# Kernel optimization log

Hardware: AMD Instinct MI355X
Metric: run time of the kernel (lower is better)

Reference implementation:

```python
import jax, jax.numpy as jnp
import numpy as np

D_MODEL = 1024
N_HEADS = 16
D_K = D_MODEL // N_HEADS
EPS = 1e-8


def _l2_rownorm(x):
    # RowNormActivation: normalize each row (last dim) to unit L2 norm
    return x * jax.lax.rsqrt(jnp.sum(x * x, axis=-1, keepdims=True) + EPS)


def setup_inputs() -> dict:
    key = jax.random.key(0)
    ks = jax.random.split(key, 11)
    B, S = 2, 2048
    sc = 1.0 / np.sqrt(D_MODEL)
    inp = {
        "Q": jax.random.normal(ks[0], (B, S, D_MODEL), jnp.float32),
        "K": jax.random.normal(ks[1], (B, S, D_MODEL), jnp.float32),
        "V": jax.random.normal(ks[2], (B, S, D_MODEL), jnp.float32),
        "Wq_w": jax.random.normal(ks[3], (D_MODEL, D_MODEL), jnp.float32) * sc,
        "Wq_b": jnp.zeros((D_MODEL,), jnp.float32),
        "Wk_w": jax.random.normal(ks[4], (D_MODEL, D_MODEL), jnp.float32) * sc,
        "Wk_b": jnp.zeros((D_MODEL,), jnp.float32),
        "Wv_w": jax.random.normal(ks[5], (D_MODEL, D_MODEL), jnp.float32) * sc,
        "Wv_b": jnp.zeros((D_MODEL,), jnp.float32),
        "Wo_w": jax.random.normal(ks[6], (D_MODEL, D_MODEL), jnp.float32) * sc,
        "Wo_b": jnp.zeros((D_MODEL,), jnp.float32),
    }
    return inp


def reference(Q, K, V, Wq_w, Wq_b, Wk_w, Wk_b, Wv_w, Wv_b, Wo_w, Wo_b):
    B, S, _ = Q.shape
    # torch Linear: y = x @ W.T + b
    q = (Q @ Wq_w.T + Wq_b).reshape(B, S, N_HEADS, D_K).transpose(0, 2, 1, 3)
    k = (K @ Wk_w.T + Wk_b).reshape(B, S, N_HEADS, D_K).transpose(0, 2, 1, 3)
    v = (V @ Wv_w.T + Wv_b).reshape(B, S, N_HEADS, D_K).transpose(0, 2, 1, 3)
    qn = _l2_rownorm(q)
    kn = _l2_rownorm(k)
    scores = jnp.einsum("bhqd,bhkd->bhqk", qn, kn)
    attn = scores * scores  # squared similarity, no softmax (dropout=0 / eval)
    out = jnp.einsum("bhqk,bhkd->bhqd", attn, v)
    out = out.transpose(0, 2, 1, 3).reshape(B, S, D_MODEL)
    return out @ Wo_w.T + Wo_b
```

## Files before the change

### kernel.cpp

```cpp
#include <hip/hip_runtime.h>


#define D_MODEL 1024
#define N_HEADS 16
#define D_K     64
#define BATCH   2
#define SEQ     2048
#define M_TOT   (BATCH * SEQ)

typedef short  s16x8 __attribute__((ext_vector_type(8)));
typedef float  f32x4 __attribute__((ext_vector_type(4)));
typedef unsigned short ushort_t;
typedef ushort_t us4 __attribute__((ext_vector_type(4)));

__device__ __forceinline__ ushort_t f2bf(float f) {
    union { float f; unsigned int u; } x; x.f = f;
    unsigned int u = x.u;
    return (ushort_t)((u + 0x7fffu + ((u >> 16) & 1u)) >> 16);
}
__device__ __forceinline__ float bf2f(ushort_t h) {
    union { unsigned int u; float f; } x; x.u = ((unsigned int)h) << 16;
    return x.f;
}

__device__ __forceinline__ void gload_lds16(const ushort_t* g, ushort_t* l) {
    __builtin_amdgcn_global_load_lds(
        (__attribute__((address_space(1))) void*)(ushort_t*)g,
        (__attribute__((address_space(3))) void*)l, 16, 0, 0);
}

#define WAIT_VM(n)  asm volatile("s_waitcnt vmcnt(" #n ")" ::: "memory")
#define WAIT_LGKM0  asm volatile("s_waitcnt lgkmcnt(0)" ::: "memory")
#define BARRIER     asm volatile("s_barrier" ::: "memory")

struct ConvArgs {
    const float* src[11];
    ushort_t*    dst[11];
    int          n[11];
};

__global__ __launch_bounds__(256) void convert_kernel(ConvArgs a) {
    const int t = blockIdx.y;
    const int i = (blockIdx.x * 256 + threadIdx.x) * 4;
    if (i >= a.n[t]) return;
    const float4 v = *(const float4*)(a.src[t] + i);
    us4 p;
    p[0] = f2bf(v.x); p[1] = f2bf(v.y); p[2] = f2bf(v.z); p[3] = f2bf(v.w);
    *(us4*)(a.dst[t] + i) = p;
}

template <int BM, int MODE>
__device__ __forceinline__ void gemm_body(
    ushort_t* __restrict__ smem,
    const ushort_t* __restrict__ A,
    const ushort_t* __restrict__ W,
    const ushort_t* __restrict__ bias,
    ushort_t* __restrict__ out,
    float* __restrict__ outf,
    int bx, int by)
{
    static_assert(BM == 64 || BM == 128, "");
    constexpr int K    = 1024;
    constexpr int MF   = BM / 32;
    constexpr int BUFW = (BM + 128) * 64;
    constexpr int NIT  = K / 64;

    const int t    = threadIdx.x;
    const int wave = t >> 6;
    const int lane = t & 63;
    const int quad = lane >> 4;
    const int lc   = lane & 15;
    const int wm   = wave >> 1;
    const int wn   = wave & 1;
    const int m0   = bx * BM;
    const int n0   = by * 128;

    f32x4 acc[MF][4];
    const f32x4 zero = {0.f, 0.f, 0.f, 0.f};
#pragma unroll
    for (int i = 0; i < MF; ++i)
#pragma unroll
        for (int j = 0; j < 4; ++j) acc[i][j] = zero;

    auto stage = [&](int buf, int k0) {
        ushort_t* Ast = smem + buf * BUFW;
        ushort_t* Bst = Ast + BM * 64;
#pragma unroll
        for (int c = 0; c < MF; ++c) {
            int idx = c * 256 + t;
            int row = idx >> 3, phys = idx & 7;
            int col = (phys ^ (row & 7)) * 8;
            gload_lds16(A + (size_t)(m0 + row) * K + k0 + col, Ast + idx * 8);
        }
#pragma unroll
        for (int c = 0; c < 4; ++c) {
            int idx = c * 256 + t;
            int row = idx >> 3, phys = idx & 7;
            int col = (phys ^ (row & 7)) * 8;
            gload_lds16(W + (size_t)(n0 + row) * K + k0 + col, Bst + idx * 8);
        }
    };
    auto comp = [&](int buf) {
        ushort_t* Ast = smem + buf * BUFW;
        ushort_t* Bst = Ast + BM * 64;
#pragma unroll
        for (int ks = 0; ks < 2; ++ks) {
            const int ph = ((ks * 4 + quad) ^ (lc & 7)) * 8;
            s16x8 a[MF], b[4];
#pragma unroll
            for (int i = 0; i < MF; ++i)
                a[i] = *(const s16x8*)(Ast + (wm * (BM / 2) + i * 16 + lc) * 64 + ph);
#pragma unroll
            for (int i = 0; i < 4; ++i)
                b[i] = *(const s16x8*)(Bst + (wn * 64 + i * 16 + lc) * 64 + ph);
#pragma unroll
            for (int mf = 0; mf < MF; ++mf)
#pragma unroll
                for (int nf = 0; nf < 4; ++nf)
                    acc[mf][nf] = __builtin_amdgcn_mfma_f32_16x16x32_bf16(
                        a[mf], b[nf], acc[mf][nf], 0, 0, 0);
        }
    };

    stage(0, 0);
    stage(1, 64);
    for (int it = 0; it < NIT - 2; ++it) {
        if constexpr (BM == 128) WAIT_VM(8); else WAIT_VM(6);
        BARRIER;
        comp(it & 1);
        WAIT_LGKM0;
        BARRIER;
        stage(it & 1, (it + 2) * 64);
    }
    if constexpr (BM == 128) WAIT_VM(8); else WAIT_VM(6);
    BARRIER;
    comp((NIT - 2) & 1);
    WAIT_VM(0);
    BARRIER;
    comp((NIT - 1) & 1);

    float bv[4];
#pragma unroll
    for (int nf = 0; nf < 4; ++nf) bv[nf] = bf2f(bias[n0 + wn * 64 + nf * 16 + lc]);

    if (MODE == 0) {
#pragma unroll
        for (int mf = 0; mf < MF; ++mf)
#pragma unroll
            for (int nf = 0; nf < 4; ++nf)
#pragma unroll
                for (int r = 0; r < 4; ++r) {
                    int mg = m0 + wm * (BM / 2) + mf * 16 + quad * 4 + r;
                    int ng = n0 + wn * 64 + nf * 16 + lc;
                    outf[(size_t)mg * D_MODEL + ng] = acc[mf][nf][r] + bv[nf];
                }
    } else if (MODE == 1) {
#pragma unroll
        for (int mf = 0; mf < MF; ++mf)
#pragma unroll
            for (int r = 0; r < 4; ++r) {
                float ss = 0.f;
#pragma unroll
                for (int nf = 0; nf < 4; ++nf) {
                    float v = acc[mf][nf][r] + bv[nf];
                    acc[mf][nf][r] = v;
                    ss += v * v;
                }
                ss += __shfl_xor(ss, 1);
                ss += __shfl_xor(ss, 2);
                ss += __shfl_xor(ss, 4);
                ss += __shfl_xor(ss, 8);
                float inv = rsqrtf(ss + 1e-8f);
                int mg = m0 + wm * (BM / 2) + mf * 16 + quad * 4 + r;
                int b  = mg >> 11;
                int s  = mg & 2047;
#pragma unroll
                for (int nf = 0; nf < 4; ++nf) {
                    int ng = n0 + wn * 64 + nf * 16 + lc;
                    int h = ng >> 6, d = ng & 63;
                    out[(((size_t)(b * N_HEADS + h)) * SEQ + s) * D_K + d] =
                        f2bf(acc[mf][nf][r] * inv);
                }
            }
    } else {
        __syncthreads();
        ushort_t* vt = smem + wave * (64 * 72);
#pragma unroll
        for (int mf = 0; mf < 4; ++mf)
#pragma unroll
            for (int nf = 0; nf < 4; ++nf) {
                us4 p;
#pragma unroll
                for (int r = 0; r < 4; ++r) p[r] = f2bf(acc[mf][nf][r] + bv[nf]);
                *(us4*)(vt + (nf * 16 + lc) * 72 + mf * 16 + quad * 4) = p;
            }
        WAIT_LGKM0;
#pragma unroll
        for (int r = 0; r < 8; ++r) {
            int d  = r * 8 + (lane >> 3);
            int so = (lane & 7) * 8;
            uint4 val = *(const uint4*)(vt + d * 72 + so);
            int mg = m0 + wm * 64 + so;
            int b  = mg >> 11;
            int s  = mg & 2047;
            int ng = n0 + wn * 64 + d;
            int h = ng >> 6, dh = ng & 63;
            *(uint4*)(out + (((size_t)(b * N_HEADS + h)) * D_K + dh) * SEQ + s) = val;
        }
    }
}

__global__ __launch_bounds__(256) void qkv_kernel(
    const ushort_t* __restrict__ Qb, const ushort_t* __restrict__ Kb,
    const ushort_t* __restrict__ Vb,
    const ushort_t* __restrict__ Wq, const ushort_t* __restrict__ Wk,
    const ushort_t* __restrict__ Wv,
    const ushort_t* __restrict__ bq, const ushort_t* __restrict__ bk,
    const ushort_t* __restrict__ bv,
    ushort_t* __restrict__ qn, ushort_t* __restrict__ kn,
    ushort_t* __restrict__ vT)
{
    __shared__ __align__(16) ushort_t smem[2 * (128 + 128) * 64];
    const int z = blockIdx.z;
    if (z == 0)
        gemm_body<128, 1>(smem, Qb, Wq, bq, qn, nullptr, blockIdx.x, blockIdx.y);
    else if (z == 1)
        gemm_body<128, 1>(smem, Kb, Wk, bk, kn, nullptr, blockIdx.x, blockIdx.y);
    else
        gemm_body<128, 2>(smem, Vb, Wv, bv, vT, nullptr, blockIdx.x, blockIdx.y);
}

__global__ __launch_bounds__(256) void wo_kernel(
    const ushort_t* __restrict__ A, const ushort_t* __restrict__ W,
    const ushort_t* __restrict__ bias, float* __restrict__ outf)
{
    __shared__ __align__(16) ushort_t smem[2 * (64 + 128) * 64];
    gemm_body<64, 0>(smem, A, W, bias, nullptr, outf, blockIdx.x, blockIdx.y);
}

__global__ __launch_bounds__(256) void attn_kernel(
    const ushort_t* __restrict__ qn,
    const ushort_t* __restrict__ kn,
    const ushort_t* __restrict__ vT,
    ushort_t* __restrict__ attn_out)
{
    __shared__ __align__(16) ushort_t smem[2 * 8192 + 4 * 16 * 72];

    const int t    = threadIdx.x;
    const int wave = t >> 6;
    const int lane = t & 63;
    const int quad = lane >> 4;
    const int lc   = lane & 15;
    const int qt   = blockIdx.x;
    const int bh   = blockIdx.y;
    const int b    = bh >> 4;
    const int h    = bh & 15;

    const ushort_t* qb = qn + (size_t)bh * SEQ * D_K;
    const ushort_t* kb = kn + (size_t)bh * SEQ * D_K;
    const ushort_t* vb = vT + (size_t)bh * D_K * SEQ;
    const int q0 = qt * 64 + wave * 16;

    s16x8 aq[2];
#pragma unroll
    for (int ks = 0; ks < 2; ++ks)
        aq[ks] = *(const s16x8*)(qb + (size_t)(q0 + lc) * D_K + ks * 32 + quad * 8);

    f32x4 oacc[4];
    const f32x4 zero = {0.f, 0.f, 0.f, 0.f};
#pragma unroll
    for (int df = 0; df < 4; ++df) oacc[df] = zero;

    ushort_t* pl = smem + 2 * 8192 + wave * 16 * 72;

    auto stage = [&](int buf, int j0) {
        ushort_t* kst = smem + buf * 8192;
        ushort_t* vst = kst + 4096;
#pragma unroll
        for (int c = 0; c < 2; ++c) {
            int idx = c * 256 + t;
            int row = idx >> 3, phys = idx & 7;
            int col = (phys ^ (row & 7)) * 8;
            gload_lds16(kb + (size_t)(j0 + row) * D_K + col, kst + idx * 8);
            gload_lds16(vb + (size_t)row * SEQ + j0 + col, vst + idx * 8);
        }
    };
    auto comp = [&](int buf) {
        ushort_t* kst = smem + buf * 8192;
        ushort_t* vst = kst + 4096;
        const int ph0 = ((0 * 4 + quad) ^ (lc & 7)) * 8;
        const int ph1 = ((1 * 4 + quad) ^ (lc & 7)) * 8;
        s16x8 bk[4][2];
#pragma unroll
        for (int jf = 0; jf < 4; ++jf) {
            bk[jf][0] = *(const s16x8*)(kst + (jf * 16 + lc) * 64 + ph0);
            bk[jf][1] = *(const s16x8*)(kst + (jf * 16 + lc) * 64 + ph1);
        }
        f32x4 s[4];
#pragma unroll
        for (int jf = 0; jf < 4; ++jf) {
            s[jf] = zero;
#pragma unroll
            for (int ks = 0; ks < 2; ++ks)
                s[jf] = __builtin_amdgcn_mfma_f32_16x16x32_bf16(aq[ks], bk[jf][ks], s[jf], 0, 0, 0);
        }
#pragma unroll
        for (int jf = 0; jf < 4; ++jf)
#pragma unroll
            for (int r = 0; r < 4; ++r)
                pl[(quad * 4 + r) * 72 + jf * 16 + lc] = f2bf(s[jf][r] * s[jf][r]);
        s16x8 bvf[4][2];
#pragma unroll
        for (int df = 0; df < 4; ++df) {
            bvf[df][0] = *(const s16x8*)(vst + (df * 16 + lc) * 64 + ph0);
            bvf[df][1] = *(const s16x8*)(vst + (df * 16 + lc) * 64 + ph1);
        }
        WAIT_LGKM0;
        s16x8 aa[2];
#pragma unroll
        for (int ks = 0; ks < 2; ++ks)
            aa[ks] = *(const s16x8*)(pl + lc * 72 + ks * 32 + quad * 8);
#pragma unroll
        for (int df = 0; df < 4; ++df)
#pragma unroll
            for (int ks = 0; ks < 2; ++ks)
                oacc[df] = __builtin_amdgcn_mfma_f32_16x16x32_bf16(
                    aa[ks], bvf[df][ks], oacc[df], 0, 0, 0);
    };

    constexpr int NT = 32;
    stage(0, 0);
    stage(1, 64);
    for (int it = 0; it < NT - 2; ++it) {
        WAIT_VM(4);
        BARRIER;
        comp(it & 1);
        WAIT_LGKM0;
        BARRIER;
        stage(it & 1, (it + 2) * 64);
    }
    WAIT_VM(4);
    BARRIER;
    comp((NT - 2) & 1);
    WAIT_VM(0);
    BARRIER;
    comp((NT - 1) & 1);

#pragma unroll
    for (int df = 0; df < 4; ++df)
#pragma unroll
        for (int r = 0; r < 4; ++r) {
            int s = q0 + quad * 4 + r;
            int d = df * 16 + lc;
            attn_out[((size_t)(b * SEQ + s)) * D_MODEL + h * D_K + d] =
                f2bf(oacc[df][r]);
        }
}

extern "C" void kernel_launch(void* const* d_in, const int* in_sizes, int n_in,
                              void* d_out, int out_size, void* d_ws, size_t ws_size,
                              hipStream_t stream)
{
    const float* Qf   = (const float*)d_in[0];
    const float* Kf   = (const float*)d_in[1];
    const float* Vf   = (const float*)d_in[2];
    const float* Wqf  = (const float*)d_in[3];
    const float* Wqbf = (const float*)d_in[4];
    const float* Wkf  = (const float*)d_in[5];
    const float* Wkbf = (const float*)d_in[6];
    const float* Wvf  = (const float*)d_in[7];
    const float* Wvbf = (const float*)d_in[8];
    const float* Wof  = (const float*)d_in[9];
    const float* Wobf = (const float*)d_in[10];

    const size_t NM = (size_t)M_TOT * D_MODEL;
    const size_t NW = (size_t)D_MODEL * D_MODEL;
    const size_t NB = D_MODEL;

    ushort_t* p = (ushort_t*)d_ws;
    ushort_t* Qb  = p;  p += NM;
    ushort_t* Kb  = p;  p += NM;
    ushort_t* Vb  = p;  p += NM;
    ushort_t* Wq  = p;  p += NW;
    ushort_t* Wk  = p;  p += NW;
    ushort_t* Wv  = p;  p += NW;
    ushort_t* Wo  = p;  p += NW;
    ushort_t* bq  = p;  p += NB;
    ushort_t* bk  = p;  p += NB;
    ushort_t* bvv = p;  p += NB;
    ushort_t* bo  = p;  p += NB;
    ushort_t* qn  = p;  p += NM;
    ushort_t* kn  = p;  p += NM;
    ushort_t* vT  = p;  p += NM;
    ushort_t* ao  = p;  p += NM;

    ConvArgs ca;
    ca.src[0] = Qf;   ca.dst[0] = Qb;  ca.n[0] = (int)NM;
    ca.src[1] = Kf;   ca.dst[1] = Kb;  ca.n[1] = (int)NM;
    ca.src[2] = Vf;   ca.dst[2] = Vb;  ca.n[2] = (int)NM;
    ca.src[3] = Wqf;  ca.dst[3] = Wq;  ca.n[3] = (int)NW;
    ca.src[4] = Wkf;  ca.dst[4] = Wk;  ca.n[4] = (int)NW;
    ca.src[5] = Wvf;  ca.dst[5] = Wv;  ca.n[5] = (int)NW;
    ca.src[6] = Wof;  ca.dst[6] = Wo;  ca.n[6] = (int)NW;
    ca.src[7] = Wqbf; ca.dst[7] = bq;  ca.n[7] = (int)NB;
    ca.src[8] = Wkbf; ca.dst[8] = bk;  ca.n[8] = (int)NB;
    ca.src[9] = Wvbf; ca.dst[9] = bvv; ca.n[9] = (int)NB;
    ca.src[10] = Wobf; ca.dst[10] = bo; ca.n[10] = (int)NB;

    dim3 blk(256);
    convert_kernel<<<dim3((unsigned)(NM / (256 * 4)), 11), blk, 0, stream>>>(ca);

    qkv_kernel<<<dim3(M_TOT / 128, D_MODEL / 128, 3), blk, 0, stream>>>(
        Qb, Kb, Vb, Wq, Wk, Wv, bq, bk, bvv, qn, kn, vT);
    attn_kernel<<<dim3(SEQ / 64, BATCH * N_HEADS), blk, 0, stream>>>(qn, kn, vT, ao);
    wo_kernel<<<dim3(M_TOT / 64, D_MODEL / 128), blk, 0, stream>>>(
        ao, Wo, bo, (float*)d_out);
}
```

Measured before the change: 238.2 us.

## Double per-wave query rows in attention and vectorize score stores

Each attention wave now handles 32 query rows instead of 16, so every K/V tile staged in shared memory is reused across twice as many queries and global K/V traffic per query is halved. The QK MFMA operands are swapped so each lane holds four consecutive key scores, which lets the squared scores be packed into bf16 pairs and written with one 8-byte store instead of scalar stores. The grid is reordered to put batch-head on x and halved along the query dimension, so there are fewer blocks, more accumulator registers per wave, and less occupancy.

After: 243.7 us. 2.3% more time.

```diff
diff --git a/kernel.cpp b/kernel.cpp
--- a/kernel.cpp
+++ b/kernel.cpp
@@ -1,4 +1,5 @@
 #include <hip/hip_runtime.h>
+#include <hip/hip_bf16.h>
 
 
 #define D_MODEL 1024
@@ -21,6 +22,11 @@
 __device__ __forceinline__ float bf2f(ushort_t h) {
     union { unsigned int u; float f; } x; x.u = ((unsigned int)h) << 16;
     return x.f;
+}
+__device__ __forceinline__ unsigned int pack2bf(float a, float b) {
+    union { __hip_bfloat162 h; unsigned int u; } x;
+    x.h = __float22bfloat162_rn(float2{a, b});
+    return x.u;
 }
 
 __device__ __forceinline__ void gload_lds16(const ushort_t* g, ushort_t* l) {
@@ -244,34 +250,39 @@
     const ushort_t* __restrict__ vT,
     ushort_t* __restrict__ attn_out)
 {
-    __shared__ __align__(16) ushort_t smem[2 * 8192 + 4 * 16 * 72];
+    __shared__ __align__(16) ushort_t smem[2 * 8192 + 4 * 32 * 72];
 
     const int t    = threadIdx.x;
     const int wave = t >> 6;
     const int lane = t & 63;
     const int quad = lane >> 4;
     const int lc   = lane & 15;
-    const int qt   = blockIdx.x;
-    const int bh   = blockIdx.y;
+    const int bh   = blockIdx.x;
+    const int qt   = blockIdx.y;
     const int b    = bh >> 4;
     const int h    = bh & 15;
 
     const ushort_t* qb = qn + (size_t)bh * SEQ * D_K;
     const ushort_t* kb = kn + (size_t)bh * SEQ * D_K;
     const ushort_t* vb = vT + (size_t)bh * D_K * SEQ;
-    const int q0 = qt * 64 + wave * 16;
-
-    s16x8 aq[2];
-#pragma unroll
-    for (int ks = 0; ks < 2; ++ks)
-        aq[ks] = *(const s16x8*)(qb + (size_t)(q0 + lc) * D_K + ks * 32 + quad * 8);
-
-    f32x4 oacc[4];
+    const int q0 = qt * 128 + wave * 32;
+
+    s16x8 aq[2][2];
+#pragma unroll
+    for (int mf = 0; mf < 2; ++mf)
+#pragma unroll
+        for (int ks = 0; ks < 2; ++ks)
+            aq[mf][ks] = *(const s16x8*)(qb + (size_t)(q0 + mf * 16 + lc) * D_K +
+                                         ks * 32 + quad * 8);
+
+    f32x4 oacc[2][4];
     const f32x4 zero = {0.f, 0.f, 0.f, 0.f};
 #pragma unroll
-    for (int df = 0; df < 4; ++df) oacc[df] = zero;
-
-    ushort_t* pl = smem + 2 * 8192 + wave * 16 * 72;
+    for (int mf = 0; mf < 2; ++mf)
+#pragma unroll
+        for (int df = 0; df < 4; ++df) oacc[mf][df] = zero;
+
+    ushort_t* pl = smem + 2 * 8192 + wave * 32 * 72;
 
     auto stage = [&](int buf, int j0) {
         ushort_t* kst = smem + buf * 8192;
@@ -296,19 +307,28 @@
             bk[jf][0] = *(const s16x8*)(kst + (jf * 16 + lc) * 64 + ph0);
             bk[jf][1] = *(const s16x8*)(kst + (jf * 16 + lc) * 64 + ph1);
         }
-        f32x4 s[4];
-#pragma unroll
-        for (int jf = 0; jf < 4; ++jf) {
-            s[jf] = zero;
-#pragma unroll
-            for (int ks = 0; ks < 2; ++ks)
-                s[jf] = __builtin_amdgcn_mfma_f32_16x16x32_bf16(aq[ks], bk[jf][ks], s[jf], 0, 0, 0);
-        }
+        f32x4 s[4][2];
 #pragma unroll
         for (int jf = 0; jf < 4; ++jf)
 #pragma unroll
-            for (int r = 0; r < 4; ++r)
-                pl[(quad * 4 + r) * 72 + jf * 16 + lc] = f2bf(s[jf][r] * s[jf][r]);
+            for (int mf = 0; mf < 2; ++mf) {
+                s[jf][mf] = zero;
+#pragma unroll
+                for (int ks = 0; ks < 2; ++ks)
+                    s[jf][mf] = __builtin_amdgcn_mfma_f32_16x16x32_bf16(
+                        bk[jf][ks], aq[mf][ks], s[jf][mf], 0, 0, 0);
+            }
+#pragma unroll
+        for (int jf = 0; jf < 4; ++jf)
+#pragma unroll
+            for (int mf = 0; mf < 2; ++mf) {
+                float p0 = s[jf][mf][0] * s[jf][mf][0];
+                float p1 = s[jf][mf][1] * s[jf][mf][1];
+                float p2 = s[jf][mf][2] * s[jf][mf][2];
+                float p3 = s[jf][mf][3] * s[jf][mf][3];
+                uint2 w = {pack2bf(p0, p1), pack2bf(p2, p3)};
+                *(uint2*)(pl + (mf * 16 + lc) * 72 + jf * 16 + quad * 4) = w;
+            }
         s16x8 bvf[4][2];
 #pragma unroll
         for (int df = 0; df < 4; ++df) {
@@ -316,16 +336,21 @@
             bvf[df][1] = *(const s16x8*)(vst + (df * 16 + lc) * 64 + ph1);
         }
         WAIT_LGKM0;
-        s16x8 aa[2];
-#pragma unroll
-        for (int ks = 0; ks < 2; ++ks)
-            aa[ks] = *(const s16x8*)(pl + lc * 72 + ks * 32 + quad * 8);
-#pragma unroll
-        for (int df = 0; df < 4; ++df)
+        s16x8 aa[2][2];
+#pragma unroll
+        for (int mf = 0; mf < 2; ++mf)
 #pragma unroll
             for (int ks = 0; ks < 2; ++ks)
-                oacc[df] = __builtin_amdgcn_mfma_f32_16x16x32_bf16(
-                    aa[ks], bvf[df][ks], oacc[df], 0, 0, 0);
+                aa[mf][ks] = *(const s16x8*)(pl + (mf * 16 + lc) * 72 +
+                                             ks * 32 + quad * 8);
+#pragma unroll
+        for (int mf = 0; mf < 2; ++mf)
+#pragma unroll
+            for (int df = 0; df < 4; ++df)
+#pragma unroll
+                for (int ks = 0; ks < 2; ++ks)
+                    oacc[mf][df] = __builtin_amdgcn_mfma_f32_16x16x32_bf16(
+                        aa[mf][ks], bvf[df][ks], oacc[mf][df], 0, 0, 0);
     };
 
     constexpr int NT = 32;
@@ -347,14 +372,16 @@
     comp((NT - 1) & 1);
 
 #pragma unroll
-    for (int df = 0; df < 4; ++df)
-#pragma unroll
-        for (int r = 0; r < 4; ++r) {
-            int s = q0 + quad * 4 + r;
-            int d = df * 16 + lc;
-            attn_out[((size_t)(b * SEQ + s)) * D_MODEL + h * D_K + d] =
-                f2bf(oacc[df][r]);
-        }
+    for (int mf = 0; mf < 2; ++mf)
+#pragma unroll
+        for (int df = 0; df < 4; ++df)
+#pragma unroll
+            for (int r = 0; r < 4; ++r) {
+                int s = q0 + mf * 16 + quad * 4 + r;
+                int d = df * 16 + lc;
+                attn_out[((size_t)(b * SEQ + s)) * D_MODEL + h * D_K + d] =
+                    f2bf(oacc[mf][df][r]);
+            }
 }
 
 extern "C" void kernel_launch(void* const* d_in, const int* in_sizes, int n_in,
@@ -412,7 +439,7 @@
 
     qkv_kernel<<<dim3(M_TOT / 128, D_MODEL / 128, 3), blk, 0, stream>>>(
         Qb, Kb, Vb, Wq, Wk, Wv, bq, bk, bvv, qn, kn, vT);
-    attn_kernel<<<dim3(SEQ / 64, BATCH * N_HEADS), blk, 0, stream>>>(qn, kn, vT, ao);
+    attn_kernel<<<dim3(BATCH * N_HEADS, SEQ / 128), blk, 0, stream>>>(qn, kn, vT, ao);
     wo_kernel<<<dim3(M_TOT / 64, D_MODEL / 128), blk, 0, stream>>>(
         ao, Wo, bo, (float*)d_out);
 }
```

## Split attention work by key columns across waves, keep scores in registers

Applied to the files above, without the earlier changes.

The attention kernel now has each wave own a 16-key slice of every staged tile for all 64 query rows, instead of each wave owning 16 query rows. Scores are computed transposed (K as the A operand), squared, and packed straight into registers as the A operand of a 16x16x16 MFMA, which removes the per-tile LDS round-trip for the probability matrix. The cost is four times as many output accumulators per wave plus a cross-wave reduction through LDS at the end. The grid is also reordered so that consecutive blocks cover different heads.

Result: no change. 237.7 us (-0.2%).

```diff
diff --git a/kernel.cpp b/kernel.cpp
--- a/kernel.cpp
+++ b/kernel.cpp
@@ -1,4 +1,5 @@
 #include <hip/hip_runtime.h>
+#include <hip/hip_bf16.h>
 
 
 #define D_MODEL 1024
@@ -9,6 +10,7 @@
 #define M_TOT   (BATCH * SEQ)
 
 typedef short  s16x8 __attribute__((ext_vector_type(8)));
+typedef short  s16x4 __attribute__((ext_vector_type(4)));
 typedef float  f32x4 __attribute__((ext_vector_type(4)));
 typedef unsigned short ushort_t;
 typedef ushort_t us4 __attribute__((ext_vector_type(4)));
@@ -22,6 +24,26 @@
     union { unsigned int u; float f; } x; x.u = ((unsigned int)h) << 16;
     return x.f;
 }
+__device__ __forceinline__ unsigned int pack2bf(float a, float b) {
+    union { __hip_bfloat162 h; unsigned int u; } x;
+    x.h = __float22bfloat162_rn(float2{a, b});
+    return x.u;
+}
+
+#if defined(__has_builtin)
+#if __has_builtin(__builtin_amdgcn_mfma_f32_16x16x16bf16_1k)
+#define MFMA16K16(a, b, c) __builtin_amdgcn_mfma_f32_16x16x16bf16_1k(a, b, c, 0, 0, 0)
+#endif
+#endif
+#ifndef MFMA16K16
+__device__ __forceinline__ f32x4 mfma16k16_asm(s16x4 a, s16x4 b, f32x4 c) {
+    f32x4 d;
+    asm volatile("v_mfma_f32_16x16x16_bf16 %0, %1, %2, %3\n\ts_nop 1"
+                 : "=v"(d) : "v"(a), "v"(b), "v"(c));
+    return d;
+}
+#define MFMA16K16(a, b, c) mfma16k16_asm(a, b, c)
+#endif
 
 __device__ __forceinline__ void gload_lds16(const ushort_t* g, ushort_t* l) {
     __builtin_amdgcn_global_load_lds(
@@ -244,34 +266,39 @@
     const ushort_t* __restrict__ vT,
     ushort_t* __restrict__ attn_out)
 {
-    __shared__ __align__(16) ushort_t smem[2 * 8192 + 4 * 16 * 72];
+    __shared__ __align__(16) ushort_t smem[2 * 8192];
+    __shared__ float red[3 * 16 * 68];
 
     const int t    = threadIdx.x;
     const int wave = t >> 6;
     const int lane = t & 63;
     const int quad = lane >> 4;
     const int lc   = lane & 15;
-    const int qt   = blockIdx.x;
-    const int bh   = blockIdx.y;
+    const int bh   = blockIdx.x;
+    const int qt   = blockIdx.y;
     const int b    = bh >> 4;
     const int h    = bh & 15;
 
     const ushort_t* qb = qn + (size_t)bh * SEQ * D_K;
     const ushort_t* kb = kn + (size_t)bh * SEQ * D_K;
     const ushort_t* vb = vT + (size_t)bh * D_K * SEQ;
-    const int q0 = qt * 64 + wave * 16;
-
-    s16x8 aq[2];
-#pragma unroll
-    for (int ks = 0; ks < 2; ++ks)
-        aq[ks] = *(const s16x8*)(qb + (size_t)(q0 + lc) * D_K + ks * 32 + quad * 8);
-
-    f32x4 oacc[4];
+    const int q0 = qt * 64;
+    const int jw = wave * 16;
+
+    s16x8 qf[4][2];
+#pragma unroll
+    for (int mf = 0; mf < 4; ++mf)
+#pragma unroll
+        for (int ks = 0; ks < 2; ++ks)
+            qf[mf][ks] = *(const s16x8*)(qb + (size_t)(q0 + mf * 16 + lc) * D_K +
+                                         ks * 32 + quad * 8);
+
+    f32x4 oacc[4][4];
     const f32x4 zero = {0.f, 0.f, 0.f, 0.f};
 #pragma unroll
-    for (int df = 0; df < 4; ++df) oacc[df] = zero;
-
-    ushort_t* pl = smem + 2 * 8192 + wave * 16 * 72;
+    for (int mf = 0; mf < 4; ++mf)
+#pragma unroll
+        for (int df = 0; df < 4; ++df) oacc[mf][df] = zero;
 
     auto stage = [&](int buf, int j0) {
         ushort_t* kst = smem + buf * 8192;
@@ -288,44 +315,31 @@
     auto comp = [&](int buf) {
         ushort_t* kst = smem + buf * 8192;
         ushort_t* vst = kst + 4096;
-        const int ph0 = ((0 * 4 + quad) ^ (lc & 7)) * 8;
-        const int ph1 = ((1 * 4 + quad) ^ (lc & 7)) * 8;
-        s16x8 bk[4][2];
-#pragma unroll
-        for (int jf = 0; jf < 4; ++jf) {
-            bk[jf][0] = *(const s16x8*)(kst + (jf * 16 + lc) * 64 + ph0);
-            bk[jf][1] = *(const s16x8*)(kst + (jf * 16 + lc) * 64 + ph1);
-        }
-        f32x4 s[4];
-#pragma unroll
-        for (int jf = 0; jf < 4; ++jf) {
-            s[jf] = zero;
+        s16x8 ak[2];
+#pragma unroll
+        for (int ks = 0; ks < 2; ++ks)
+            ak[ks] = *(const s16x8*)(kst + (jw + lc) * 64 +
+                                     (((ks * 4 + quad) ^ (lc & 7)) * 8));
+        s16x4 bv4[4];
+#pragma unroll
+        for (int df = 0; df < 4; ++df) {
+            int row = df * 16 + lc;
+            int chk = (wave * 2 + (quad >> 1)) ^ (row & 7);
+            bv4[df] = *(const s16x4*)(vst + row * 64 + chk * 8 + (quad & 1) * 4);
+        }
+#pragma unroll
+        for (int mf = 0; mf < 4; ++mf) {
+            f32x4 st = zero;
 #pragma unroll
             for (int ks = 0; ks < 2; ++ks)
-                s[jf] = __builtin_amdgcn_mfma_f32_16x16x32_bf16(aq[ks], bk[jf][ks], s[jf], 0, 0, 0);
-        }
-#pragma unroll
-        for (int jf = 0; jf < 4; ++jf)
-#pragma unroll
-            for (int r = 0; r < 4; ++r)
-                pl[(quad * 4 + r) * 72 + jf * 16 + lc] = f2bf(s[jf][r] * s[jf][r]);
-        s16x8 bvf[4][2];
-#pragma unroll
-        for (int df = 0; df < 4; ++df) {
-            bvf[df][0] = *(const s16x8*)(vst + (df * 16 + lc) * 64 + ph0);
-            bvf[df][1] = *(const s16x8*)(vst + (df * 16 + lc) * 64 + ph1);
-        }
-        WAIT_LGKM0;
-        s16x8 aa[2];
-#pragma unroll
-        for (int ks = 0; ks < 2; ++ks)
-            aa[ks] = *(const s16x8*)(pl + lc * 72 + ks * 32 + quad * 8);
-#pragma unroll
-        for (int df = 0; df < 4; ++df)
-#pragma unroll
-            for (int ks = 0; ks < 2; ++ks)
-                oacc[df] = __builtin_amdgcn_mfma_f32_16x16x32_bf16(
-                    aa[ks], bvf[df][ks], oacc[df], 0, 0, 0);
+                st = __builtin_amdgcn_mfma_f32_16x16x32_bf16(ak[ks], qf[mf][ks], st, 0, 0, 0);
+            union { unsigned int u[2]; s16x4 v; } pa;
+            pa.u[0] = pack2bf(st[0] * st[0], st[1] * st[1]);
+            pa.u[1] = pack2bf(st[2] * st[2], st[3] * st[3]);
+#pragma unroll
+            for (int df = 0; df < 4; ++df)
+                oacc[mf][df] = MFMA16K16(pa.v, bv4[df], oacc[mf][df]);
+        }
     };
 
     constexpr int NT = 32;
@@ -346,15 +360,35 @@
     BARRIER;
     comp((NT - 1) & 1);
 
-#pragma unroll
-    for (int df = 0; df < 4; ++df)
-#pragma unroll
-        for (int r = 0; r < 4; ++r) {
-            int s = q0 + quad * 4 + r;
-            int d = df * 16 + lc;
-            attn_out[((size_t)(b * SEQ + s)) * D_MODEL + h * D_K + d] =
-                f2bf(oacc[df][r]);
-        }
+    __syncthreads();
+#pragma unroll
+    for (int c = 0; c < 4; ++c) {
+        if (wave != c) {
+            int widx = wave - (wave > c ? 1 : 0);
+#pragma unroll
+            for (int df = 0; df < 4; ++df)
+#pragma unroll
+                for (int r = 0; r < 4; ++r)
+                    red[widx * (16 * 68) + (quad * 4 + r) * 68 + df * 16 + lc] =
+                        oacc[c][df][r];
+        }
+        __syncthreads();
+        if (wave == c) {
+#pragma unroll
+            for (int df = 0; df < 4; ++df)
+#pragma unroll
+                for (int r = 0; r < 4; ++r) {
+                    float v = oacc[c][df][r];
+#pragma unroll
+                    for (int w2 = 0; w2 < 3; ++w2)
+                        v += red[w2 * (16 * 68) + (quad * 4 + r) * 68 + df * 16 + lc];
+                    int s = q0 + c * 16 + quad * 4 + r;
+                    int d = df * 16 + lc;
+                    attn_out[((size_t)(b * SEQ + s)) * D_MODEL + h * D_K + d] = f2bf(v);
+                }
+        }
+        __syncthreads();
+    }
 }
 
 extern "C" void kernel_launch(void* const* d_in, const int* in_sizes, int n_in,
@@ -412,7 +446,7 @@
 
     qkv_kernel<<<dim3(M_TOT / 128, D_MODEL / 128, 3), blk, 0, stream>>>(
         Qb, Kb, Vb, Wq, Wk, Wv, bq, bk, bvv, qn, kn, vT);
-    attn_kernel<<<dim3(SEQ / 64, BATCH * N_HEADS), blk, 0, stream>>>(qn, kn, vT, ao);
+    attn_kernel<<<dim3(BATCH * N_HEADS, SEQ / 64), blk, 0, stream>>>(qn, kn, vT, ao);
     wo_kernel<<<dim3(M_TOT / 64, D_MODEL / 128), blk, 0, stream>>>(
         ao, Wo, bo, (float*)d_out);
 }
```
